# Optimization experiments

Hardware: AMD Instinct MI355X
Metric: run time of the kernel (lower is better)

The kernel has to match this reference:

```python
import jax, jax.numpy as jnp
import numpy as np
import math

B, SQ, SK = 8, 1024, 1024
DQ = DK = DV = 1024
H = 16
EPS = 1e-5


def _layer_norm(x, g, b):
    mu = jnp.mean(x, axis=-1, keepdims=True)
    var = jnp.mean(jnp.square(x - mu), axis=-1, keepdims=True)
    return (x - mu) * jax.lax.rsqrt(var + EPS) * g + b


def setup_inputs() -> dict:
    key = jax.random.key(0)
    ks = jax.random.split(key, 8)
    s_q = 1.0 / math.sqrt(DQ)
    s_v = 1.0 / math.sqrt(DV)
    return {
        "Q": jax.random.normal(ks[0], (B, SQ, DQ), dtype=jnp.float32),
        "K": jax.random.normal(ks[1], (B, SK, DK), dtype=jnp.float32),
        "Wq": jax.random.normal(ks[2], (DQ, DV), dtype=jnp.float32) * s_q,
        "bq": jnp.zeros((DV,), dtype=jnp.float32),
        "Wk": jax.random.normal(ks[3], (DK, DV), dtype=jnp.float32) * s_q,
        "bk": jnp.zeros((DV,), dtype=jnp.float32),
        "Wv": jax.random.normal(ks[4], (DK, DV), dtype=jnp.float32) * s_q,
        "bv": jnp.zeros((DV,), dtype=jnp.float32),
        "Wo": jax.random.normal(ks[5], (DV, DV), dtype=jnp.float32) * s_v,
        "bo": jnp.zeros((DV,), dtype=jnp.float32),
        "g0": jnp.ones((DV,), dtype=jnp.float32),
        "b0": jnp.zeros((DV,), dtype=jnp.float32),
        "g1": jnp.ones((DV,), dtype=jnp.float32),
        "b1": jnp.zeros((DV,), dtype=jnp.float32),
    }


def reference(Q, K, Wq, bq, Wk, bk, Wv, bv, Wo, bo, g0, b0, g1, b1):
    dh = DV // H
    q = Q @ Wq + bq                      # [B,SQ,DV]
    k = K @ Wk + bk                      # [B,SK,DV]
    v = K @ Wv + bv                      # [B,SK,DV]
    # split/cat over heads == reshape to [B,S,H,dh]
    qh = q.reshape(B, SQ, H, dh)
    kh = k.reshape(B, SK, H, dh)
    vh = v.reshape(B, SK, H, dh)
    # NOTE: original scales by sqrt(dim_V), not sqrt(head_dim)
    scores = jnp.einsum("bqhd,bkhd->bhqk", qh, kh) / math.sqrt(DV)
    A = jax.nn.softmax(scores, axis=-1)  # [B,H,SQ,SK]
    attn = jnp.einsum("bhqk,bkhd->bqhd", A, vh)
    out = q + attn.reshape(B, SQ, DV)    # residual with projected Q
    out = _layer_norm(out, g0, b0)
    out = out + jax.nn.relu(out @ Wo + bo)
    out = _layer_norm(out, g1, b1)
    return out
```

## Files before the change

kernel.cpp:

```cpp
#include <hip/hip_runtime.h>
#include <hip/hip_bf16.h>
#include <stdint.h>

#define NB 8
#define NSQ 1024
#define NSK 1024
#define ND 1024
#define NH 16
#define NDH 64
#define NM (NB * NSQ)
#define LOG2E 1.4426950408889634f

typedef __bf16 bf16;
typedef __bf16 bf16x8 __attribute__((ext_vector_type(8)));
typedef float f32x4 __attribute__((ext_vector_type(4)));
typedef float f32x16 __attribute__((ext_vector_type(16)));
typedef unsigned int uint32;

__device__ __forceinline__ void async_load16(const void* g, void* l) {
  __builtin_amdgcn_global_load_lds(
      (__attribute__((address_space(1))) void*)g,
      (__attribute__((address_space(3))) void*)l, 16, 0, 0);
}

__device__ __forceinline__ void permswap(uint32& x, uint32& y) {
#if __has_builtin(__builtin_amdgcn_permlane32_swap)
  auto r = __builtin_amdgcn_permlane32_swap(x, y, false, false);
  x = r[0]; y = r[1];
#else
  asm volatile("v_permlane32_swap_b32 %0, %1" : "+v"(x), "+v"(y));
#endif
}

__global__ __launch_bounds__(256) void cvt_f32_bf16(const float* __restrict__ in,
                                                    bf16* __restrict__ out, int n4) {
  int i = blockIdx.x * 256 + threadIdx.x;
  if (i < n4) {
    float4 v = *(const float4*)(in + (size_t)i * 4);
    union { uint64_t u; bf16 h[4]; } o;
    o.h[0] = (bf16)v.x; o.h[1] = (bf16)v.y; o.h[2] = (bf16)v.z; o.h[3] = (bf16)v.w;
    *(uint64_t*)(out + (size_t)i * 4) = o.u;
  }
}

__global__ __launch_bounds__(256) void transpose_cvt(const float* __restrict__ W,
                                                     bf16* __restrict__ Wt) {
  __shared__ float t[64][65];
  const int bc = blockIdx.x * 64;
  const int br = blockIdx.y * 64;
  const int tid = threadIdx.x;
  for (int c = tid; c < 1024; c += 256) {
    int r = c >> 4, off = (c & 15) * 4;
    float4 v = *(const float4*)&W[(size_t)(br + r) * 1024 + bc + off];
    t[r][off] = v.x; t[r][off + 1] = v.y; t[r][off + 2] = v.z; t[r][off + 3] = v.w;
  }
  __syncthreads();
  for (int c = tid; c < 512; c += 256) {
    int cc = c >> 3, rr = (c & 7) * 8;
    union { uint4 u; bf16 h[8]; } o;
#pragma unroll
    for (int i = 0; i < 8; ++i) o.h[i] = (bf16)t[rr + i][cc];
    *(uint4*)&Wt[(size_t)(bc + cc) * 1024 + br + rr] = o.u;
  }
}

__global__ __launch_bounds__(256) void transpose_v(const bf16* __restrict__ vsrc,
                                                   bf16* __restrict__ vT) {
  const int st = blockIdx.x * 64;
  const int bh = blockIdx.y;
  const int b = bh >> 4, h = bh & 15;
  __shared__ __align__(16) bf16 t[64][72];
  const int tid = threadIdx.x;
  for (int c = tid; c < 512; c += 256) {
    int s = c >> 3, off = (c & 7) * 8;
    *(uint4*)&t[s][off] =
        *(const uint4*)&vsrc[(size_t)(b * NSK + st + s) * 2048 + 1024 + h * NDH + off];
  }
  __syncthreads();
  for (int c = tid; c < 512; c += 256) {
    int d = c >> 3, s0 = (c & 7) * 8;
    union { uint4 u; bf16 h[8]; } o;
#pragma unroll
    for (int i = 0; i < 8; ++i) o.h[i] = t[s0 + i][d];
    *(uint4*)&vT[((size_t)(bh * NDH + d)) * NSK + st + s0] = o.u;
  }
}

template <int BM, int MODE, int NX>
__global__ __launch_bounds__(512, 2) void gemm8p(
    const bf16* __restrict__ A, const bf16* __restrict__ Bt,
    const float* __restrict__ bias, const float* __restrict__ bias2,
    bf16* __restrict__ Cb, const bf16* __restrict__ Resb, float scale, int N) {
  constexpr int RA = BM / 64;
  constexpr int NT = 16;
  constexpr int MR = BM / 32;
  __shared__ __align__(16) bf16 As[2][BM * 64];
  __shared__ __align__(16) bf16 Bs[2][256 * 64];

  const int tid = threadIdx.x;
  const int flat = blockIdx.x;
  const int nwg = gridDim.x;
  const int xi = (flat & 7) * (nwg >> 3) + (flat >> 3);
  const int bcol = (xi & (NX - 1)) * 256;
  const int brow = (xi / NX) * BM;

  const int w = tid >> 6, lane = tid & 63;
  const int wm = w >> 2, wn = w & 3;
  const int lr = lane & 15, l4 = lane >> 4;
  const int rgrp = l4 * 4;
  const int rk = lr & 7;

  const int rowoff = tid >> 3;
  const int gsrc = (tid & 7) ^ ((tid >> 3) & 7);
  const bf16* Ag = A + (size_t)(brow + rowoff) * 1024 + gsrc * 8;
  const bf16* Bg = Bt + (size_t)(bcol + rowoff) * 1024 + gsrc * 8;
  const int lds_o = rowoff * 64 + (tid & 7) * 8;

  auto stA = [&](int d, int r, int kt) {
    async_load16(Ag + (size_t)r * (64 * 1024) + kt * 64, &As[d][r * 4096 + lds_o]);
  };
  auto stB = [&](int d, int r, int kt) {
    async_load16(Bg + (size_t)r * (64 * 1024) + kt * 64, &Bs[d][r * 4096 + lds_o]);
  };
  auto fA = [&](int d, int mrow, int ks) {
    return *(const bf16x8*)&As[d][(mrow + lr) * 64 + (((ks * 4 + l4) ^ rk) * 8)];
  };
  auto fB = [&](int d, int nrow, int ks) {
    return *(const bf16x8*)&Bs[d][(nrow + lr) * 64 + (((ks * 4 + l4) ^ rk) * 8)];
  };

  f32x4 acc[MR][4] = {};
  bf16x8 af[4][2], bfr[4][2];

#pragma unroll
  for (int r = 0; r < RA; ++r) stA(0, r, 0);
#pragma unroll
  for (int r = 0; r < 4; ++r) stB(0, r, 0);
  stA(1, 0, 1);
  stA(1, 1, 1);
  asm volatile("s_waitcnt vmcnt(2)" ::: "memory");
  __builtin_amdgcn_s_barrier();

  for (int t = 0; t < NT; ++t) {
    const int cur = t & 1, nxt = cur ^ 1;
#pragma unroll
    for (int i = 0; i < 4; ++i) {
      af[i][0] = fA(cur, wm * (BM / 2) + i * 16, 0);
      af[i][1] = fA(cur, wm * (BM / 2) + i * 16, 1);
    }
#pragma unroll
    for (int j = 0; j < 2; ++j) {
      bfr[j][0] = fB(cur, wn * 64 + j * 16, 0);
      bfr[j][1] = fB(cur, wn * 64 + j * 16, 1);
    }
    if (t + 1 < NT) {
      if constexpr (BM == 256) { stA(nxt, 2, t + 1); stA(nxt, 3, t + 1); }
      else                     { stB(nxt, 0, t + 1); stB(nxt, 1, t + 1); }
    }
    __builtin_amdgcn_s_barrier();
    asm volatile("s_waitcnt lgkmcnt(0)" ::: "memory");
    __builtin_amdgcn_sched_barrier(0);
    __builtin_amdgcn_s_setprio(1);
    if constexpr (BM == 256) {
#pragma unroll
      for (int i = 0; i < 4; ++i)
#pragma unroll
        for (int j = 0; j < 2; ++j)
#pragma unroll
          for (int ks = 0; ks < 2; ++ks)
            acc[i][j] = __builtin_amdgcn_mfma_f32_16x16x32_bf16(af[i][ks], bfr[j][ks], acc[i][j], 0, 0, 0);
    } else {
#pragma unroll
      for (int i = 0; i < 4; ++i)
#pragma unroll
        for (int ks = 0; ks < 2; ++ks)
          acc[i][0] = __builtin_amdgcn_mfma_f32_16x16x32_bf16(af[i][ks], bfr[0][ks], acc[i][0], 0, 0, 0);
    }
    __builtin_amdgcn_s_setprio(0);
    __builtin_amdgcn_s_barrier();
#pragma unroll
    for (int j = 2; j < 4; ++j) {
      bfr[j][0] = fB(cur, wn * 64 + j * 16, 0);
      bfr[j][1] = fB(cur, wn * 64 + j * 16, 1);
    }
    if (t + 1 < NT) {
      if constexpr (BM == 256) { stB(nxt, 0, t + 1); stB(nxt, 1, t + 1); }
      else                     { stB(nxt, 2, t + 1); stB(nxt, 3, t + 1); }
    }
    __builtin_amdgcn_s_barrier();
    asm volatile("s_waitcnt lgkmcnt(0)" ::: "memory");
    __builtin_amdgcn_sched_barrier(0);
    __builtin_amdgcn_s_setprio(1);
    if constexpr (BM == 256) {
#pragma unroll
      for (int i = 0; i < 4; ++i)
#pragma unroll
        for (int j = 2; j < 4; ++j)
#pragma unroll
          for (int ks = 0; ks < 2; ++ks)
            acc[i][j] = __builtin_amdgcn_mfma_f32_16x16x32_bf16(af[i][ks], bfr[j][ks], acc[i][j], 0, 0, 0);
    } else {
#pragma unroll
      for (int i = 0; i < 4; ++i)
#pragma unroll
        for (int ks = 0; ks < 2; ++ks)
          acc[i][1] = __builtin_amdgcn_mfma_f32_16x16x32_bf16(af[i][ks], bfr[1][ks], acc[i][1], 0, 0, 0);
    }
    __builtin_amdgcn_s_setprio(0);
    __builtin_amdgcn_s_barrier();
    if constexpr (BM == 256) {
#pragma unroll
      for (int i = 0; i < 4; ++i) {
        af[i][0] = fA(cur, wm * 128 + 64 + i * 16, 0);
        af[i][1] = fA(cur, wm * 128 + 64 + i * 16, 1);
      }
      if (t + 1 < NT) { stB(nxt, 2, t + 1); stB(nxt, 3, t + 1); }
    }
    __builtin_amdgcn_s_barrier();
    if constexpr (BM == 256) {
      asm volatile("s_waitcnt lgkmcnt(0)" ::: "memory");
      __builtin_amdgcn_sched_barrier(0);
    }
    __builtin_amdgcn_s_setprio(1);
    if constexpr (BM == 256) {
#pragma unroll
      for (int i = 0; i < 4; ++i)
#pragma unroll
        for (int j = 0; j < 2; ++j)
#pragma unroll
          for (int ks = 0; ks < 2; ++ks)
            acc[4 + i][j] = __builtin_amdgcn_mfma_f32_16x16x32_bf16(af[i][ks], bfr[j][ks], acc[4 + i][j], 0, 0, 0);
    } else {
#pragma unroll
      for (int i = 0; i < 4; ++i)
#pragma unroll
        for (int ks = 0; ks < 2; ++ks)
          acc[i][2] = __builtin_amdgcn_mfma_f32_16x16x32_bf16(af[i][ks], bfr[2][ks], acc[i][2], 0, 0, 0);
    }
    __builtin_amdgcn_s_setprio(0);
    __builtin_amdgcn_s_barrier();
    if (t + 2 < NT) { stA(cur, 0, t + 2); stA(cur, 1, t + 2); }
    __builtin_amdgcn_s_barrier();
    __builtin_amdgcn_s_setprio(1);
    if constexpr (BM == 256) {
#pragma unroll
      for (int i = 0; i < 4; ++i)
#pragma unroll
        for (int j = 2; j < 4; ++j)
#pragma unroll
          for (int ks = 0; ks < 2; ++ks)
            acc[4 + i][j] = __builtin_amdgcn_mfma_f32_16x16x32_bf16(af[i][ks], bfr[j][ks], acc[4 + i][j], 0, 0, 0);
    } else {
#pragma unroll
      for (int i = 0; i < 4; ++i)
#pragma unroll
        for (int ks = 0; ks < 2; ++ks)
          acc[i][3] = __builtin_amdgcn_mfma_f32_16x16x32_bf16(af[i][ks], bfr[3][ks], acc[i][3], 0, 0, 0);
    }
    __builtin_amdgcn_s_setprio(0);
    if (t + 1 < NT) {
      if (t + 2 < NT) asm volatile("s_waitcnt vmcnt(2)" ::: "memory");
      else            asm volatile("s_waitcnt vmcnt(0)" ::: "memory");
    }
    __builtin_amdgcn_s_barrier();
  }

#pragma unroll
  for (int m = 0; m < MR; ++m) {
#pragma unroll
    for (int n = 0; n < 4; ++n) {
      const int col = bcol + wn * 64 + n * 16 + lr;
      float bv, sc;
      if (MODE == 2) {
        const bool isV = (bcol >= 1024);
        bv = isV ? bias2[col - 1024] : bias[col];
        sc = isV ? 1.0f : LOG2E;
      } else {
        bv = bias[col];
        sc = scale;
      }
#pragma unroll
      for (int r = 0; r < 4; ++r) {
        const int row = brow + wm * (BM / 2) + m * 16 + rgrp + r;
        float v = acc[m][n][r] + bv;
        if (MODE == 1) {
          float res = (float)Resb[(size_t)row * N + col];
          Cb[(size_t)row * N + col] = (bf16)(res + (v > 0.f ? v : 0.f));
        } else {
          Cb[(size_t)row * N + col] = (bf16)(v * sc);
        }
      }
    }
  }
}

__global__ __launch_bounds__(256, 2) void attn_kernel(
    const bf16* __restrict__ qb, const bf16* __restrict__ kvb,
    const bf16* __restrict__ vT, bf16* __restrict__ attnout) {
  const int bh = blockIdx.y;
  const int b = bh >> 4, h = bh & 15;
  const int tid = threadIdx.x, w = tid >> 6, lane = tid & 63;
  const int l31 = lane & 31;
  const int l1 = lane >> 5;
  const int q0w = blockIdx.x * 256 + w * 64;

  __shared__ __align__(16) bf16 Kl[2][64 * 64];
  __shared__ __align__(16) bf16 Vl[2][64 * 64];

  const int srow = w * 8 + (lane >> 3);
  const int gsw = (lane & 7) ^ (lane >> 3);
  const int rg = l31 & 7;

  const bf16* kbase = kvb + (size_t)(b * NSK) * 2048 + h * NDH;
  const bf16* vbase = vT + (size_t)(bh * NDH) * NSK;

  bf16x8 qf[2][4];
#pragma unroll
  for (int qs = 0; qs < 2; ++qs)
#pragma unroll
    for (int kd = 0; kd < 4; ++kd)
      qf[qs][kd] = *(const bf16x8*)&qb[(size_t)(b * NSQ + q0w + qs * 32 + l31) * ND +
                                       h * NDH + kd * 16 + l1 * 8];

  f32x16 oacc[2][2] = {};
  f32x16 lacc[2] = {};
  bf16x8 ones;
#pragma unroll
  for (int i = 0; i < 8; ++i) ones[i] = (bf16)1.0f;

  auto stage = [&](int bi, int kt) {
    async_load16(kbase + (size_t)(kt + srow) * 2048 + gsw * 8, &Kl[bi][w * 512]);
    async_load16(kbase + (size_t)(kt + 32 + srow) * 2048 + gsw * 8, &Kl[bi][2048 + w * 512]);
    async_load16(vbase + (size_t)srow * NSK + kt + gsw * 8, &Vl[bi][w * 512]);
    async_load16(vbase + (size_t)(32 + srow) * NSK + kt + gsw * 8, &Vl[bi][2048 + w * 512]);
  };

  stage(0, 0);

  for (int t = 0; t < 16; ++t) {
    const int bi = t & 1;
    asm volatile("s_waitcnt vmcnt(0)" ::: "memory");
    __syncthreads();
    if (t < 15) stage(bi ^ 1, (t + 1) * 64);

    bf16x8 kf[2][4];
#pragma unroll
    for (int n = 0; n < 2; ++n)
#pragma unroll
      for (int kd = 0; kd < 4; ++kd)
        kf[n][kd] = *(const bf16x8*)&Kl[bi][(n * 32 + l31) * 64 + (((kd * 2 + l1) ^ rg) * 8)];

    bf16x8 pa[2][4];
#pragma unroll
    for (int qs = 0; qs < 2; ++qs) {
      f32x16 s0 = {}, s1 = {};
      __builtin_amdgcn_s_setprio(1);
#pragma unroll
      for (int kd = 0; kd < 4; ++kd) {
        s0 = __builtin_amdgcn_mfma_f32_32x32x16_bf16(kf[0][kd], qf[qs][kd], s0, 0, 0, 0);
        s1 = __builtin_amdgcn_mfma_f32_32x32x16_bf16(kf[1][kd], qf[qs][kd], s1, 0, 0, 0);
      }
      __builtin_amdgcn_s_setprio(0);
      float e0[16], e1[16];
#pragma unroll
      for (int r = 0; r < 16; ++r) {
        e0[r] = __builtin_amdgcn_exp2f(s0[r]);
        e1[r] = __builtin_amdgcn_exp2f(s1[r]);
      }
      uint32 W[2][4][2];
#pragma unroll
      for (int r2 = 0; r2 < 4; ++r2)
#pragma unroll
        for (int p = 0; p < 2; ++p) {
          uint32 w0, w1;
          asm("v_cvt_pk_bf16_f32 %0, %1, %2"
              : "=v"(w0) : "v"(e0[r2 * 4 + 2 * p]), "v"(e0[r2 * 4 + 2 * p + 1]));
          asm("v_cvt_pk_bf16_f32 %0, %1, %2"
              : "=v"(w1) : "v"(e1[r2 * 4 + 2 * p]), "v"(e1[r2 * 4 + 2 * p + 1]));
          W[0][r2][p] = w0; W[1][r2][p] = w1;
        }
#pragma unroll
      for (int kc = 0; kc < 4; ++kc) {
        uint32 x0 = W[kc >> 1][(kc & 1) * 2][0], y0 = W[kc >> 1][(kc & 1) * 2 + 1][0];
        uint32 x1 = W[kc >> 1][(kc & 1) * 2][1], y1 = W[kc >> 1][(kc & 1) * 2 + 1][1];
        permswap(x0, y0);
        permswap(x1, y1);
        union { uint32 u[4]; bf16x8 v; } cvt;
        cvt.u[0] = x0; cvt.u[1] = x1; cvt.u[2] = y0; cvt.u[3] = y1;
        pa[qs][kc] = cvt.v;
      }
    }

    bf16x8 vf[2][4];
#pragma unroll
    for (int dd = 0; dd < 2; ++dd)
#pragma unroll
      for (int kc = 0; kc < 4; ++kc)
        vf[dd][kc] = *(const bf16x8*)&Vl[bi][(dd * 32 + l31) * 64 + (((kc * 2 + l1) ^ rg) * 8)];

    __builtin_amdgcn_s_setprio(1);
#pragma unroll
    for (int qs = 0; qs < 2; ++qs)
#pragma unroll
      for (int kc = 0; kc < 4; ++kc) {
        oacc[qs][0] = __builtin_amdgcn_mfma_f32_32x32x16_bf16(pa[qs][kc], vf[0][kc], oacc[qs][0], 0, 0, 0);
        oacc[qs][1] = __builtin_amdgcn_mfma_f32_32x32x16_bf16(pa[qs][kc], vf[1][kc], oacc[qs][1], 0, 0, 0);
        lacc[qs] = __builtin_amdgcn_mfma_f32_32x32x16_bf16(pa[qs][kc], ones, lacc[qs], 0, 0, 0);
      }
    __builtin_amdgcn_s_setprio(0);
  }

#pragma unroll
  for (int qs = 0; qs < 2; ++qs) {
    float inv[16];
#pragma unroll
    for (int r = 0; r < 16; ++r) inv[r] = 1.0f / lacc[qs][r];
#pragma unroll
    for (int dd = 0; dd < 2; ++dd)
#pragma unroll
      for (int r = 0; r < 16; ++r) {
        const int row = q0w + qs * 32 + (r & 3) + 8 * (r >> 2) + 4 * l1;
        attnout[(size_t)(b * NSQ + row) * ND + h * NDH + dd * 32 + l31] =
            (bf16)(oacc[qs][dd][r] * inv[r]);
      }
  }
}

template <bool RES, bool OUTF>
__global__ __launch_bounds__(256) void ln_kernel(
    const bf16* __restrict__ x, const bf16* __restrict__ rq, float rscale,
    const float* __restrict__ g, const float* __restrict__ be,
    bf16* __restrict__ yb, float* __restrict__ yf) {
  __shared__ float sm[4];
  const int row = blockIdx.x, tid = threadIdx.x;
  const size_t base = (size_t)row * ND + tid * 4;
  union { uint2 u; bf16 h[4]; } xv;
  xv.u = *(const uint2*)(x + base);
  float v0 = (float)xv.h[0], v1 = (float)xv.h[1], v2 = (float)xv.h[2], v3 = (float)xv.h[3];
  if (RES) {
    union { uint2 u; bf16 h[4]; } q;
    q.u = *(const uint2*)(rq + base);
    v0 += rscale * (float)q.h[0]; v1 += rscale * (float)q.h[1];
    v2 += rscale * (float)q.h[2]; v3 += rscale * (float)q.h[3];
  }
  float s = v0 + v1 + v2 + v3;
#pragma unroll
  for (int off = 32; off > 0; off >>= 1) s += __shfl_down(s, off, 64);
  if ((tid & 63) == 0) sm[tid >> 6] = s;
  __syncthreads();
  const float mean = (sm[0] + sm[1] + sm[2] + sm[3]) * (1.0f / ND);
  __syncthreads();
  const float d0 = v0 - mean, d1 = v1 - mean, d2 = v2 - mean, d3 = v3 - mean;
  float sq = d0 * d0 + d1 * d1 + d2 * d2 + d3 * d3;
#pragma unroll
  for (int off = 32; off > 0; off >>= 1) sq += __shfl_down(sq, off, 64);
  if ((tid & 63) == 0) sm[tid >> 6] = sq;
  __syncthreads();
  const float var = (sm[0] + sm[1] + sm[2] + sm[3]) * (1.0f / ND);
  const float rs = rsqrtf(var + 1e-5f);
  float4 gv = *(const float4*)(g + tid * 4);
  float4 bv = *(const float4*)(be + tid * 4);
  const float y0 = d0 * rs * gv.x + bv.x;
  const float y1 = d1 * rs * gv.y + bv.y;
  const float y2 = d2 * rs * gv.z + bv.z;
  const float y3 = d3 * rs * gv.w + bv.w;
  if (OUTF) {
    *(float4*)(yf + base) = make_float4(y0, y1, y2, y3);
  } else {
    union { uint2 u; bf16 h[4]; } o;
    o.h[0] = (bf16)y0; o.h[1] = (bf16)y1; o.h[2] = (bf16)y2; o.h[3] = (bf16)y3;
    *(uint2*)(yb + base) = o.u;
  }
}

extern "C" void kernel_launch(void* const* d_in, const int* in_sizes, int n_in,
                              void* d_out, int out_size, void* d_ws, size_t ws_size,
                              hipStream_t stream) {
  const float* Q  = (const float*)d_in[0];
  const float* K  = (const float*)d_in[1];
  const float* Wq = (const float*)d_in[2];
  const float* bq = (const float*)d_in[3];
  const float* Wk = (const float*)d_in[4];
  const float* bk = (const float*)d_in[5];
  const float* Wv = (const float*)d_in[6];
  const float* bv = (const float*)d_in[7];
  const float* Wo = (const float*)d_in[8];
  const float* bo = (const float*)d_in[9];
  const float* g0 = (const float*)d_in[10];
  const float* b0 = (const float*)d_in[11];
  const float* g1 = (const float*)d_in[12];
  const float* b1 = (const float*)d_in[13];
  float* out = (float*)d_out;

  char* ws = (char*)d_ws;
  const size_t MB = 1024 * 1024;
  bf16* Qb    = (bf16*)(ws + 0);
  bf16* Kb    = (bf16*)(ws + 16 * MB);
  bf16* Wqt   = (bf16*)(ws + 32 * MB);
  bf16* Wkvt  = (bf16*)(ws + 34 * MB);
  bf16* Wot   = (bf16*)(ws + 38 * MB);
  bf16* qb    = (bf16*)(ws + 40 * MB);
  bf16* kvb   = (bf16*)(ws + 56 * MB);
  bf16* vT    = (bf16*)(ws + 88 * MB);
  bf16* attnb = (bf16*)(ws + 104 * MB);
  bf16* h0b   = (bf16*)(ws + 56 * MB);
  bf16* out1b = (bf16*)(ws + 0);

  cvt_f32_bf16<<<8192, 256, 0, stream>>>(Q, Qb, 2097152);
  cvt_f32_bf16<<<8192, 256, 0, stream>>>(K, Kb, 2097152);
  dim3 tg(16, 16);
  transpose_cvt<<<tg, 256, 0, stream>>>(Wq, Wqt);
  transpose_cvt<<<tg, 256, 0, stream>>>(Wk, Wkvt);
  transpose_cvt<<<tg, 256, 0, stream>>>(Wv, Wkvt + 1024 * 1024);
  transpose_cvt<<<tg, 256, 0, stream>>>(Wo, Wot);
  gemm8p<256, 2, 8><<<256, 512, 0, stream>>>(Kb, Wkvt, bk, bv, kvb, nullptr, 1.0f, 2048);
  gemm8p<128, 0, 4><<<256, 512, 0, stream>>>(Qb, Wqt, bq, nullptr, qb, nullptr, 0.03125f, 1024);
  transpose_v<<<dim3(16, 128), 256, 0, stream>>>(kvb, vT);
  attn_kernel<<<dim3(4, 128), 256, 0, stream>>>(qb, kvb, vT, attnb);
  ln_kernel<true, false><<<8192, 256, 0, stream>>>(attnb, qb, 32.0f, g0, b0, h0b, nullptr);
  gemm8p<128, 1, 4><<<256, 512, 0, stream>>>(h0b, Wot, bo, nullptr, out1b, h0b, 1.0f, 1024);
  ln_kernel<false, true><<<8192, 256, 0, stream>>>(out1b, nullptr, 0.f, g1, b1, nullptr, out);
}
```

Measured before the change: 195.0 us.

## Double attention waves per block with 32 query rows each, batch prep kernels

The attention kernel moves from 4 waves of 64 query rows to 8 waves of 32 rows per 256-query block. This roughly halves per-wave accumulator and fragment registers so that more waves can be resident (launch bounds 512,4), which should hide latency better. K and V fragments are now read from LDS inside the MFMA loops rather than preloaded, and the staging loads are split across 512 threads. The prep step also fuses the two f32-to-bf16 conversions and the four weight transposes into one launch each, cutting launch overhead. The cost is that each K/V tile in LDS is shared by more waves, so LDS reads per MFMA roughly double.

```diff
diff --git a/kernel.cpp b/kernel.cpp
--- a/kernel.cpp
+++ b/kernel.cpp
@@ -32,19 +32,31 @@
 #endif
 }
 
-__global__ __launch_bounds__(256) void cvt_f32_bf16(const float* __restrict__ in,
-                                                    bf16* __restrict__ out, int n4) {
+__global__ __launch_bounds__(256) void cvt2_f32_bf16(const float* __restrict__ A,
+                                                     const float* __restrict__ B,
+                                                     bf16* __restrict__ Oa,
+                                                     bf16* __restrict__ Ob) {
+  const float* in = blockIdx.y ? B : A;
+  bf16* out = blockIdx.y ? Ob : Oa;
   int i = blockIdx.x * 256 + threadIdx.x;
-  if (i < n4) {
-    float4 v = *(const float4*)(in + (size_t)i * 4);
-    union { uint64_t u; bf16 h[4]; } o;
-    o.h[0] = (bf16)v.x; o.h[1] = (bf16)v.y; o.h[2] = (bf16)v.z; o.h[3] = (bf16)v.w;
-    *(uint64_t*)(out + (size_t)i * 4) = o.u;
-  }
-}
-
-__global__ __launch_bounds__(256) void transpose_cvt(const float* __restrict__ W,
-                                                     bf16* __restrict__ Wt) {
+  float4 v = *(const float4*)(in + (size_t)i * 4);
+  union { uint64_t u; bf16 h[4]; } o;
+  o.h[0] = (bf16)v.x; o.h[1] = (bf16)v.y; o.h[2] = (bf16)v.z; o.h[3] = (bf16)v.w;
+  *(uint64_t*)(out + (size_t)i * 4) = o.u;
+}
+
+__global__ __launch_bounds__(256) void transpose_cvt4(
+    const float* __restrict__ W0, const float* __restrict__ W1,
+    const float* __restrict__ W2, const float* __restrict__ W3,
+    bf16* __restrict__ O0, bf16* __restrict__ O1,
+    bf16* __restrict__ O2, bf16* __restrict__ O3) {
+  const float* W; bf16* Wt;
+  switch (blockIdx.z) {
+    case 0: W = W0; Wt = O0; break;
+    case 1: W = W1; Wt = O1; break;
+    case 2: W = W2; Wt = O2; break;
+    default: W = W3; Wt = O3; break;
+  }
   __shared__ float t[64][65];
   const int bc = blockIdx.x * 64;
   const int br = blockIdx.y * 64;
@@ -294,7 +306,7 @@
   }
 }
 
-__global__ __launch_bounds__(256, 2) void attn_kernel(
+__global__ __launch_bounds__(512, 4) void attn_kernel(
     const bf16* __restrict__ qb, const bf16* __restrict__ kvb,
     const bf16* __restrict__ vT, bf16* __restrict__ attnout) {
   const int bh = blockIdx.y;
@@ -302,37 +314,34 @@
   const int tid = threadIdx.x, w = tid >> 6, lane = tid & 63;
   const int l31 = lane & 31;
   const int l1 = lane >> 5;
-  const int q0w = blockIdx.x * 256 + w * 64;
+  const int q0w = blockIdx.x * 256 + w * 32;
 
   __shared__ __align__(16) bf16 Kl[2][64 * 64];
   __shared__ __align__(16) bf16 Vl[2][64 * 64];
 
-  const int srow = w * 8 + (lane >> 3);
-  const int gsw = (lane & 7) ^ (lane >> 3);
+  const int srow = tid >> 3;
+  const int sgran = tid & 7;
+  const int gsw = sgran ^ (srow & 7);
+  const int ldst = srow * 64 + sgran * 8;
   const int rg = l31 & 7;
 
   const bf16* kbase = kvb + (size_t)(b * NSK) * 2048 + h * NDH;
   const bf16* vbase = vT + (size_t)(bh * NDH) * NSK;
 
-  bf16x8 qf[2][4];
-#pragma unroll
-  for (int qs = 0; qs < 2; ++qs)
-#pragma unroll
-    for (int kd = 0; kd < 4; ++kd)
-      qf[qs][kd] = *(const bf16x8*)&qb[(size_t)(b * NSQ + q0w + qs * 32 + l31) * ND +
-                                       h * NDH + kd * 16 + l1 * 8];
-
-  f32x16 oacc[2][2] = {};
-  f32x16 lacc[2] = {};
+  bf16x8 qf[4];
+#pragma unroll
+  for (int kd = 0; kd < 4; ++kd)
+    qf[kd] = *(const bf16x8*)&qb[(size_t)(b * NSQ + q0w + l31) * ND +
+                                 h * NDH + kd * 16 + l1 * 8];
+
+  f32x16 oacc0 = {}, oacc1 = {}, lacc = {};
   bf16x8 ones;
 #pragma unroll
   for (int i = 0; i < 8; ++i) ones[i] = (bf16)1.0f;
 
   auto stage = [&](int bi, int kt) {
-    async_load16(kbase + (size_t)(kt + srow) * 2048 + gsw * 8, &Kl[bi][w * 512]);
-    async_load16(kbase + (size_t)(kt + 32 + srow) * 2048 + gsw * 8, &Kl[bi][2048 + w * 512]);
-    async_load16(vbase + (size_t)srow * NSK + kt + gsw * 8, &Vl[bi][w * 512]);
-    async_load16(vbase + (size_t)(32 + srow) * NSK + kt + gsw * 8, &Vl[bi][2048 + w * 512]);
+    async_load16(kbase + (size_t)(kt + srow) * 2048 + gsw * 8, &Kl[bi][ldst]);
+    async_load16(vbase + (size_t)srow * NSK + kt + gsw * 8, &Vl[bi][ldst]);
   };
 
   stage(0, 0);
@@ -343,86 +352,55 @@
     __syncthreads();
     if (t < 15) stage(bi ^ 1, (t + 1) * 64);
 
-    bf16x8 kf[2][4];
-#pragma unroll
-    for (int n = 0; n < 2; ++n)
-#pragma unroll
-      for (int kd = 0; kd < 4; ++kd)
-        kf[n][kd] = *(const bf16x8*)&Kl[bi][(n * 32 + l31) * 64 + (((kd * 2 + l1) ^ rg) * 8)];
-
-    bf16x8 pa[2][4];
-#pragma unroll
-    for (int qs = 0; qs < 2; ++qs) {
-      f32x16 s0 = {}, s1 = {};
+    uint32 W[2][4][2];
+#pragma unroll
+    for (int n = 0; n < 2; ++n) {
+      f32x16 s = {};
       __builtin_amdgcn_s_setprio(1);
 #pragma unroll
       for (int kd = 0; kd < 4; ++kd) {
-        s0 = __builtin_amdgcn_mfma_f32_32x32x16_bf16(kf[0][kd], qf[qs][kd], s0, 0, 0, 0);
-        s1 = __builtin_amdgcn_mfma_f32_32x32x16_bf16(kf[1][kd], qf[qs][kd], s1, 0, 0, 0);
+        bf16x8 kf = *(const bf16x8*)&Kl[bi][(n * 32 + l31) * 64 + (((kd * 2 + l1) ^ rg) * 8)];
+        s = __builtin_amdgcn_mfma_f32_32x32x16_bf16(kf, qf[kd], s, 0, 0, 0);
       }
       __builtin_amdgcn_s_setprio(0);
-      float e0[16], e1[16];
-#pragma unroll
-      for (int r = 0; r < 16; ++r) {
-        e0[r] = __builtin_amdgcn_exp2f(s0[r]);
-        e1[r] = __builtin_amdgcn_exp2f(s1[r]);
-      }
-      uint32 W[2][4][2];
 #pragma unroll
       for (int r2 = 0; r2 < 4; ++r2)
 #pragma unroll
         for (int p = 0; p < 2; ++p) {
-          uint32 w0, w1;
-          asm("v_cvt_pk_bf16_f32 %0, %1, %2"
-              : "=v"(w0) : "v"(e0[r2 * 4 + 2 * p]), "v"(e0[r2 * 4 + 2 * p + 1]));
-          asm("v_cvt_pk_bf16_f32 %0, %1, %2"
-              : "=v"(w1) : "v"(e1[r2 * 4 + 2 * p]), "v"(e1[r2 * 4 + 2 * p + 1]));
-          W[0][r2][p] = w0; W[1][r2][p] = w1;
+          float elo = __builtin_amdgcn_exp2f(s[r2 * 4 + 2 * p]);
+          float ehi = __builtin_amdgcn_exp2f(s[r2 * 4 + 2 * p + 1]);
+          uint32 wd;
+          asm("v_cvt_pk_bf16_f32 %0, %1, %2" : "=v"(wd) : "v"(elo), "v"(ehi));
+          W[n][r2][p] = wd;
         }
-#pragma unroll
-      for (int kc = 0; kc < 4; ++kc) {
-        uint32 x0 = W[kc >> 1][(kc & 1) * 2][0], y0 = W[kc >> 1][(kc & 1) * 2 + 1][0];
-        uint32 x1 = W[kc >> 1][(kc & 1) * 2][1], y1 = W[kc >> 1][(kc & 1) * 2 + 1][1];
-        permswap(x0, y0);
-        permswap(x1, y1);
-        union { uint32 u[4]; bf16x8 v; } cvt;
-        cvt.u[0] = x0; cvt.u[1] = x1; cvt.u[2] = y0; cvt.u[3] = y1;
-        pa[qs][kc] = cvt.v;
-      }
-    }
-
-    bf16x8 vf[2][4];
-#pragma unroll
-    for (int dd = 0; dd < 2; ++dd)
-#pragma unroll
-      for (int kc = 0; kc < 4; ++kc)
-        vf[dd][kc] = *(const bf16x8*)&Vl[bi][(dd * 32 + l31) * 64 + (((kc * 2 + l1) ^ rg) * 8)];
-
+    }
     __builtin_amdgcn_s_setprio(1);
 #pragma unroll
-    for (int qs = 0; qs < 2; ++qs)
-#pragma unroll
-      for (int kc = 0; kc < 4; ++kc) {
-        oacc[qs][0] = __builtin_amdgcn_mfma_f32_32x32x16_bf16(pa[qs][kc], vf[0][kc], oacc[qs][0], 0, 0, 0);
-        oacc[qs][1] = __builtin_amdgcn_mfma_f32_32x32x16_bf16(pa[qs][kc], vf[1][kc], oacc[qs][1], 0, 0, 0);
-        lacc[qs] = __builtin_amdgcn_mfma_f32_32x32x16_bf16(pa[qs][kc], ones, lacc[qs], 0, 0, 0);
-      }
+    for (int kc = 0; kc < 4; ++kc) {
+      uint32 x0 = W[kc >> 1][(kc & 1) * 2][0], y0 = W[kc >> 1][(kc & 1) * 2 + 1][0];
+      uint32 x1 = W[kc >> 1][(kc & 1) * 2][1], y1 = W[kc >> 1][(kc & 1) * 2 + 1][1];
+      permswap(x0, y0);
+      permswap(x1, y1);
+      union { uint32 u[4]; bf16x8 v; } cvt;
+      cvt.u[0] = x0; cvt.u[1] = x1; cvt.u[2] = y0; cvt.u[3] = y1;
+      bf16x8 pa = cvt.v;
+      bf16x8 vf0 = *(const bf16x8*)&Vl[bi][(l31) * 64 + (((kc * 2 + l1) ^ rg) * 8)];
+      bf16x8 vf1 = *(const bf16x8*)&Vl[bi][(32 + l31) * 64 + (((kc * 2 + l1) ^ rg) * 8)];
+      oacc0 = __builtin_amdgcn_mfma_f32_32x32x16_bf16(pa, vf0, oacc0, 0, 0, 0);
+      oacc1 = __builtin_amdgcn_mfma_f32_32x32x16_bf16(pa, vf1, oacc1, 0, 0, 0);
+      lacc = __builtin_amdgcn_mfma_f32_32x32x16_bf16(pa, ones, lacc, 0, 0, 0);
+    }
     __builtin_amdgcn_s_setprio(0);
   }
 
-#pragma unroll
-  for (int qs = 0; qs < 2; ++qs) {
-    float inv[16];
-#pragma unroll
-    for (int r = 0; r < 16; ++r) inv[r] = 1.0f / lacc[qs][r];
-#pragma unroll
-    for (int dd = 0; dd < 2; ++dd)
-#pragma unroll
-      for (int r = 0; r < 16; ++r) {
-        const int row = q0w + qs * 32 + (r & 3) + 8 * (r >> 2) + 4 * l1;
-        attnout[(size_t)(b * NSQ + row) * ND + h * NDH + dd * 32 + l31] =
-            (bf16)(oacc[qs][dd][r] * inv[r]);
-      }
+  float inv[16];
+#pragma unroll
+  for (int r = 0; r < 16; ++r) inv[r] = 1.0f / lacc[r];
+#pragma unroll
+  for (int r = 0; r < 16; ++r) {
+    const int row = q0w + (r & 3) + 8 * (r >> 2) + 4 * l1;
+    attnout[(size_t)(b * NSQ + row) * ND + h * NDH + l31] = (bf16)(oacc0[r] * inv[r]);
+    attnout[(size_t)(b * NSQ + row) * ND + h * NDH + 32 + l31] = (bf16)(oacc1[r] * inv[r]);
   }
 }
 
@@ -506,17 +484,13 @@
   bf16* h0b   = (bf16*)(ws + 56 * MB);
   bf16* out1b = (bf16*)(ws + 0);
 
-  cvt_f32_bf16<<<8192, 256, 0, stream>>>(Q, Qb, 2097152);
-  cvt_f32_bf16<<<8192, 256, 0, stream>>>(K, Kb, 2097152);
-  dim3 tg(16, 16);
-  transpose_cvt<<<tg, 256, 0, stream>>>(Wq, Wqt);
-  transpose_cvt<<<tg, 256, 0, stream>>>(Wk, Wkvt);
-  transpose_cvt<<<tg, 256, 0, stream>>>(Wv, Wkvt + 1024 * 1024);
-  transpose_cvt<<<tg, 256, 0, stream>>>(Wo, Wot);
+  cvt2_f32_bf16<<<dim3(8192, 2), 256, 0, stream>>>(Q, K, Qb, Kb);
+  transpose_cvt4<<<dim3(16, 16, 4), 256, 0, stream>>>(
+      Wq, Wk, Wv, Wo, Wqt, Wkvt, Wkvt + 1024 * 1024, Wot);
   gemm8p<256, 2, 8><<<256, 512, 0, stream>>>(Kb, Wkvt, bk, bv, kvb, nullptr, 1.0f, 2048);
   gemm8p<128, 0, 4><<<256, 512, 0, stream>>>(Qb, Wqt, bq, nullptr, qb, nullptr, 0.03125f, 1024);
   transpose_v<<<dim3(16, 128), 256, 0, stream>>>(kvb, vT);
-  attn_kernel<<<dim3(4, 128), 256, 0, stream>>>(qb, kvb, vT, attnb);
+  attn_kernel<<<dim3(4, 128), 512, 0, stream>>>(qb, kvb, vT, attnb);
   ln_kernel<true, false><<<8192, 256, 0, stream>>>(attnb, qb, 32.0f, g0, b0, h0b, nullptr);
   gemm8p<128, 1, 4><<<256, 512, 0, stream>>>(h0b, Wot, bo, nullptr, out1b, h0b, 1.0f, 1024);
   ln_kernel<false, true><<<8192, 256, 0, stream>>>(out1b, nullptr, 0.f, g1, b1, nullptr, out);
```

Result: faster. 182.1 us (-6.6%).
